# Performance work log

Measured on AMD Instinct MI355X. Metric: run time of the kernel, lower is better.

The kernel has to match this reference:

```python
import jax, jax.numpy as jnp
import numpy as np

N = 100000      # nodes
E = 1600000     # edges (avg degree 16)
IN = 512        # input feature dim
H, C = 8, 8     # conv1: 8 heads x 8 channels (hardcoded in module)
HID = H * C     # 64
OUT = 64        # output classes (conv2: 1 head, no concat)
NEG_SLOPE = 0.2 # PyG GATConv default leaky-relu slope


def setup_inputs() -> dict:
    key = jax.random.key(0)
    ks = jax.random.split(key, 10)
    x = jax.random.normal(ks[0], (N, IN), dtype=jnp.float32)
    edge_index = jax.random.randint(ks[1], (2, E), 0, N, dtype=jnp.int32)
    W1 = jax.random.normal(ks[2], (IN, HID), dtype=jnp.float32) / np.sqrt(IN).astype(np.float32)
    a_src1 = jax.random.normal(ks[3], (H, C), dtype=jnp.float32) * 0.1
    a_dst1 = jax.random.normal(ks[4], (H, C), dtype=jnp.float32) * 0.1
    b1 = jnp.zeros((HID,), dtype=jnp.float32)
    W2 = jax.random.normal(ks[5], (HID, OUT), dtype=jnp.float32) / np.sqrt(HID).astype(np.float32)
    a_src2 = jax.random.normal(ks[6], (1, OUT), dtype=jnp.float32) * 0.1
    a_dst2 = jax.random.normal(ks[7], (1, OUT), dtype=jnp.float32) * 0.1
    b2 = jnp.zeros((OUT,), dtype=jnp.float32)
    return {"x": x, "edge_index": edge_index, "W1": W1, "a_src1": a_src1,
            "a_dst1": a_dst1, "b1": b1, "W2": W2, "a_src2": a_src2,
            "a_dst2": a_dst2, "b2": b2}


def _gat_attend(h, src, dst, a_s, a_d, n_nodes):
    """h: [N,H,C]; src/dst: [E]; a_s/a_d: [H,C] -> aggregated [N,H,C]."""
    # per-node half-scores (PyG decomposition of a^T [Wx_i || Wx_j])
    sc_s = jnp.sum(h * a_s, axis=-1)                       # [N,H]
    sc_d = jnp.sum(h * a_d, axis=-1)                       # [N,H]
    logits = jax.nn.leaky_relu(sc_s[src] + sc_d[dst], NEG_SLOPE)  # [E,H]
    # segment softmax over edges grouped by destination node
    mx = jax.ops.segment_max(logits, dst, num_segments=n_nodes)   # [N,H]
    ex = jnp.exp(logits - mx[dst])                          # [E,H]
    denom = jax.ops.segment_sum(ex, dst, num_segments=n_nodes)    # [N,H]
    alpha = ex / (denom[dst] + 1e-16)                       # [E,H]
    msg = h[src] * alpha[:, :, None]                        # [E,H,C]
    return jax.ops.segment_sum(msg, dst, num_segments=n_nodes)    # [N,H,C]


def reference(x, edge_index, W1, a_src1, a_dst1, b1, W2, a_src2, a_dst2, b2):
    n = x.shape[0]
    loop = jnp.arange(n, dtype=edge_index.dtype)
    src = jnp.concatenate([edge_index[0], loop])            # self-loops (PyG default)
    dst = jnp.concatenate([edge_index[1], loop])
    # conv1: 8 heads, concat
    h1 = (x @ W1).reshape(n, H, C)
    o1 = _gat_attend(h1, src, dst, a_src1, a_dst1, n).reshape(n, HID) + b1
    x2 = jax.nn.elu(o1)
    # conv2: 1 head, no concat
    h2 = (x2 @ W2).reshape(n, 1, OUT)
    o2 = _gat_attend(h2, src, dst, a_src2, a_dst2, n)[:, 0] + b2
    return jax.nn.log_softmax(o2, axis=1)
```

## Files before the change

### kernel.cpp

```cpp
#include <hip/hip_runtime.h>
#include <cstdint>
#include <cstddef>

#define LEAKY 0.2f
#define NEG_INF -3.402823466e38f
static const int CHUNK = 2048;

typedef __attribute__((ext_vector_type(8))) short short8;
typedef __attribute__((ext_vector_type(4))) float floatx4;

__device__ __forceinline__ float dot4(float4 a, float4 b) {
    return a.x * b.x + a.y * b.y + a.z * b.z + a.w * b.w;
}

__device__ __forceinline__ unsigned short f2bf(float f) {
    unsigned u = __float_as_uint(f);
    u += 0x7fffu + ((u >> 16) & 1u);
    return (unsigned short)(u >> 16);
}
__device__ __forceinline__ float bf2f(unsigned short u) {
    return __uint_as_float(((unsigned)u) << 16);
}

__global__ __launch_bounds__(256) void k_init_deg(int* __restrict__ deg, int Nn) {
    int i = blockIdx.x * 256 + threadIdx.x;
    if (i < Nn) deg[i] = 1;
}

__global__ __launch_bounds__(256) void k_count_p(const int* __restrict__ ei, int* __restrict__ deg,
                                                 int E, int Nn) {
    int part = blockIdx.x & 7;
    int lo = (int)((long long)Nn * part >> 3);
    int hi = (int)((long long)Nn * (part + 1) >> 3);
    int nthr = (gridDim.x >> 3) * 256;
    int tid = (blockIdx.x >> 3) * 256 + threadIdx.x;
    for (int e = tid; e < E; e += nthr) {
        int d = ei[E + e];
        if (d >= lo && d < hi) atomicAdd(&deg[d], 1);
    }
}

__global__ __launch_bounds__(256) void k_scan1(const int* __restrict__ deg, int* __restrict__ bsum, int Nn) {
    __shared__ int sm[256];
    int b = blockIdx.x, t = threadIdx.x;
    int s = 0;
    int i0 = b * CHUNK + t * 8;
#pragma unroll
    for (int j = 0; j < 8; ++j) { int i = i0 + j; if (i < Nn) s += deg[i]; }
    sm[t] = s;
    __syncthreads();
    for (int o = 128; o; o >>= 1) { if (t < o) sm[t] += sm[t + o]; __syncthreads(); }
    if (t == 0) bsum[b] = sm[0];
}

__global__ void k_scan2(const int* __restrict__ bsum, int* __restrict__ bpre, int B) {
    int l = threadIdx.x;
    int v = (l < B) ? bsum[l] : 0;
    int inc = v;
#pragma unroll
    for (int o = 1; o < 64; o <<= 1) { int u = __shfl_up(inc, o); if (l >= o) inc += u; }
    if (l < B) bpre[l] = inc - v;
}

__global__ __launch_bounds__(256) void k_scan3(const int* __restrict__ deg, const int* __restrict__ bpre,
                                               int* __restrict__ indptr, int* __restrict__ cursor, int Nn) {
    __shared__ int wsum[4];
    int b = blockIdx.x, t = threadIdx.x, lane = t & 63, w = t >> 6;
    int i0 = b * CHUNK + t * 8;
    int d[8]; int s = 0;
#pragma unroll
    for (int j = 0; j < 8; ++j) { int i = i0 + j; d[j] = (i < Nn) ? deg[i] : 0; s += d[j]; }
    int inc = s;
#pragma unroll
    for (int o = 1; o < 64; o <<= 1) { int u = __shfl_up(inc, o); if (lane >= o) inc += u; }
    if (lane == 63) wsum[w] = inc;
    __syncthreads();
    int wofs = 0;
    for (int k = 0; k < w; ++k) wofs += wsum[k];
    int base = bpre[b] + wofs + (inc - s);
    int run = 0;
#pragma unroll
    for (int j = 0; j < 8; ++j) {
        int i = i0 + j;
        if (i < Nn) {
            int v = base + run;
            indptr[i] = v; cursor[i] = v;
            run += d[j];
            if (i == Nn - 1) indptr[Nn] = v + d[j];
        }
    }
}

__global__ __launch_bounds__(256) void k_fill_p(const int* __restrict__ ei, int* __restrict__ cursor,
                                                int* __restrict__ csr, int E, int Nn) {
    int part = blockIdx.x & 7;
    int lo = (int)((long long)Nn * part >> 3);
    int hi = (int)((long long)Nn * (part + 1) >> 3);
    int nthr = (gridDim.x >> 3) * 256;
    int tid = (blockIdx.x >> 3) * 256 + threadIdx.x;
    int tot = E + Nn;
    for (int idx = tid; idx < tot; idx += nthr) {
        int d = (idx < E) ? ei[E + idx] : idx - E;
        if (d >= lo && d < hi) {
            int s = (idx < E) ? ei[idx] : idx - E;
            int slot = atomicAdd(&cursor[d], 1);
            csr[slot] = s;
        }
    }
}

__global__ __launch_bounds__(256) void k_prepW(const float* __restrict__ W1, unsigned short* __restrict__ W1t) {
    int i = blockIdx.x * 256 + threadIdx.x;
    if (i >= 64 * 512) return;
    int n = i >> 9, k = i & 511;
    W1t[i] = f2bf(W1[k * 64 + n]);
}

__global__ __launch_bounds__(256) void gemm1_mfma(const float* __restrict__ A, const unsigned short* __restrict__ W1t,
                                                  unsigned short* __restrict__ C, int M) {
    __shared__ __align__(16) unsigned short As[128][40];
    __shared__ __align__(16) unsigned short Bs[64][40];
    int t = threadIdx.x;
    int w = t >> 6, l = t & 63;
    int quad = l >> 4, lm = l & 15;
    int row0 = blockIdx.x * 128;

    floatx4 acc[2][4] = {};

    for (int k0 = 0; k0 < 512; k0 += 32) {
#pragma unroll
        for (int j = 0; j < 4; ++j) {
            int f = t + 256 * j;
            int r = f >> 3, c4 = f & 7;
            int rg = row0 + r; if (rg >= M) rg = M - 1;
            float4 v = *(const float4*)(A + (size_t)rg * 512 + k0 + c4 * 4);
            ushort4 b; b.x = f2bf(v.x); b.y = f2bf(v.y); b.z = f2bf(v.z); b.w = f2bf(v.w);
            *(ushort4*)&As[r][c4 * 4] = b;
        }
        {
            int n = t >> 2, seg = t & 3;
            *(uint4*)&Bs[n][seg * 8] = *(const uint4*)(W1t + (size_t)n * 512 + k0 + seg * 8);
        }
        __syncthreads();

        short8 af[2], bfm[4];
#pragma unroll
        for (int tm = 0; tm < 2; ++tm) {
            int m = w * 32 + tm * 16 + lm;
            af[tm] = *(const short8*)&As[m][quad * 8];
        }
#pragma unroll
        for (int tn = 0; tn < 4; ++tn) {
            int n = tn * 16 + lm;
            bfm[tn] = *(const short8*)&Bs[n][quad * 8];
        }
#pragma unroll
        for (int tm = 0; tm < 2; ++tm)
#pragma unroll
            for (int tn = 0; tn < 4; ++tn)
                acc[tm][tn] = __builtin_amdgcn_mfma_f32_16x16x32_bf16(af[tm], bfm[tn], acc[tm][tn], 0, 0, 0);
        __syncthreads();
    }

#pragma unroll
    for (int tm = 0; tm < 2; ++tm) {
#pragma unroll
        for (int r = 0; r < 4; ++r) {
            int row = row0 + w * 32 + tm * 16 + quad * 4 + r;
            if (row < M) {
#pragma unroll
                for (int tn = 0; tn < 4; ++tn)
                    C[(size_t)row * 64 + tn * 16 + lm] = f2bf(acc[tm][tn][r]);
            }
        }
    }
}

template <int KB>
__global__ __launch_bounds__(256) void gemm_n64(const float* __restrict__ A, const float* __restrict__ B,
                                                unsigned short* __restrict__ C, int M, int K) {
    __shared__ float As[KB][68];
    __shared__ float Bs[KB][68];
    int tid = threadIdx.x;
    int row0 = blockIdx.x * 64;
    int tx = tid & 15, ty = tid >> 4;
    float acc[4][4] = {};
    for (int k0 = 0; k0 < K; k0 += KB) {
#pragma unroll
        for (int j = 0; j < (64 * KB) / (256 * 4); ++j) {
            int f = tid + 256 * j;
            int r = f / (KB / 4);
            int c4 = f % (KB / 4);
            int rg = row0 + r; if (rg >= M) rg = M - 1;
            float4 v = *(const float4*)(A + (size_t)rg * K + k0 + c4 * 4);
            As[c4 * 4 + 0][r] = v.x; As[c4 * 4 + 1][r] = v.y;
            As[c4 * 4 + 2][r] = v.z; As[c4 * 4 + 3][r] = v.w;
        }
#pragma unroll
        for (int j = 0; j < (KB * 64) / (256 * 4); ++j) {
            int f = tid + 256 * j;
            int kk = f / 16, c4 = f % 16;
            *(float4*)&Bs[kk][c4 * 4] = *(const float4*)(B + (size_t)(k0 + kk) * 64 + c4 * 4);
        }
        __syncthreads();
#pragma unroll
        for (int kk = 0; kk < KB; ++kk) {
            float4 a = *(const float4*)&As[kk][ty * 4];
            float4 b = *(const float4*)&Bs[kk][tx * 4];
            float av[4] = {a.x, a.y, a.z, a.w};
            float bv[4] = {b.x, b.y, b.z, b.w};
#pragma unroll
            for (int i = 0; i < 4; ++i)
#pragma unroll
                for (int j = 0; j < 4; ++j) acc[i][j] += av[i] * bv[j];
        }
        __syncthreads();
    }
#pragma unroll
    for (int i = 0; i < 4; ++i) {
        int rg = row0 + ty * 4 + i;
        if (rg < M) {
            ushort4 b; b.x = f2bf(acc[i][0]); b.y = f2bf(acc[i][1]);
            b.z = f2bf(acc[i][2]); b.w = f2bf(acc[i][3]);
            *(ushort4*)(C + (size_t)rg * 64 + tx * 4) = b;
        }
    }
}

__global__ __launch_bounds__(256) void k_sc1(const unsigned short* __restrict__ h1, const float* __restrict__ as1,
                                             const float* __restrict__ ad1, float* __restrict__ scs,
                                             float* __restrict__ scd, int Nn) {
    int i = blockIdx.x * 256 + threadIdx.x;
    if (i >= Nn * 8) return;
    int h = i & 7;
    ushort4 p0 = *(const ushort4*)(h1 + (size_t)i * 8);
    ushort4 p1 = *(const ushort4*)(h1 + (size_t)i * 8 + 4);
    float4 v0 = make_float4(bf2f(p0.x), bf2f(p0.y), bf2f(p0.z), bf2f(p0.w));
    float4 v1 = make_float4(bf2f(p1.x), bf2f(p1.y), bf2f(p1.z), bf2f(p1.w));
    const float4* asp = (const float4*)(as1 + h * 8);
    const float4* adp = (const float4*)(ad1 + h * 8);
    scs[i] = dot4(v0, asp[0]) + dot4(v1, asp[1]);
    scd[i] = dot4(v0, adp[0]) + dot4(v1, adp[1]);
}

__global__ __launch_bounds__(256) void k_sc2(const unsigned short* __restrict__ h2, const float* __restrict__ as2,
                                             const float* __restrict__ ad2, float* __restrict__ scs,
                                             float* __restrict__ scd, int Nn) {
    int wave = (blockIdx.x * 256 + threadIdx.x) >> 6;
    int lane = threadIdx.x & 63;
    if (wave >= Nn) return;
    float v = bf2f(h2[(size_t)wave * 64 + lane]);
    float ss = v * as2[lane], sd = v * ad2[lane];
#pragma unroll
    for (int o = 32; o; o >>= 1) { ss += __shfl_xor(ss, o); sd += __shfl_xor(sd, o); }
    if (lane == 0) { scs[wave] = ss; scd[wave] = sd; }
}

__global__ __launch_bounds__(256) void k_agg1(const unsigned short* __restrict__ h1, const float* __restrict__ scs,
                                              const float* __restrict__ scd, const int* __restrict__ indptr,
                                              const int* __restrict__ csr, const float* __restrict__ b1,
                                              float* __restrict__ x2, int Nn) {
    int node = (blockIdx.x * 256 + threadIdx.x) >> 6;
    int l = threadIdx.x & 63;
    if (node >= Nn) return;
    int h8 = l & 7, grp = l >> 3;
    int sub = l >> 5, c2 = l & 31;
    int head2 = c2 >> 2;
    int start = indptr[node], end = indptr[node + 1];
    float sd = scd[node * 8 + h8];

    float mx = NEG_INF;
    for (int base = start; base < end; base += 8) {
        int slot = base + grp;
        int s = csr[slot < end ? slot : start];
        float v = scs[s * 8 + h8] + sd;
        v = v > 0.f ? v : LEAKY * v;
        mx = fmaxf(mx, (slot < end) ? v : NEG_INF);
    }
#pragma unroll
    for (int o = 8; o < 64; o <<= 1) mx = fmaxf(mx, __shfl_xor(mx, o));

    float dsum = 0.f, acc0 = 0.f, acc1 = 0.f;
    for (int base = start; base < end; base += 64) {
        int e = base + l;
        int s64 = csr[e < end ? e : start];
        int cnt = min(64, end - base);
        int nb = (cnt + 7) >> 3;
        for (int b = 0; b < nb; ++b) {
            int slot = base + b * 8 + grp;
            int sb = __shfl(s64, b * 8 + grp);
            float v = scs[sb * 8 + h8] + sd;
            v = v > 0.f ? v : LEAKY * v;
            float ex = (slot < end) ? __expf(v - mx) : 0.f;
            dsum += ex;
#pragma unroll
            for (int j = 0; j < 8; j += 2) {
                int jj = j + sub;
                float exv = __shfl(ex, (jj << 3) | head2);
                int s = __shfl(s64, b * 8 + jj);
                unsigned hp = *(const unsigned*)(h1 + (size_t)s * 64 + c2 * 2);
                acc0 += exv * bf2f((unsigned short)(hp & 0xffffu));
                acc1 += exv * bf2f((unsigned short)(hp >> 16));
            }
        }
    }
#pragma unroll
    for (int o = 8; o < 64; o <<= 1) dsum += __shfl_xor(dsum, o);
    acc0 += __shfl_xor(acc0, 32);
    acc1 += __shfl_xor(acc1, 32);
    float dh = __shfl(dsum, head2);
    float inv = 1.f / (dh + 1e-16f);

    float o0 = acc0 * inv + b1[c2 * 2];
    float o1 = acc1 * inv + b1[c2 * 2 + 1];
    o0 = o0 > 0.f ? o0 : expm1f(o0);
    o1 = o1 > 0.f ? o1 : expm1f(o1);
    if (sub == 0) {
        float2 r = make_float2(o0, o1);
        *(float2*)&x2[(size_t)node * 64 + c2 * 2] = r;
    }
}

__global__ __launch_bounds__(256) void k_agg2(const unsigned short* __restrict__ h2, const float* __restrict__ scs,
                                              const float* __restrict__ scd, const int* __restrict__ indptr,
                                              const int* __restrict__ csr, const float* __restrict__ b2,
                                              float* __restrict__ out, int Nn) {
    int node = (blockIdx.x * 256 + threadIdx.x) >> 6;
    int l = threadIdx.x & 63;
    if (node >= Nn) return;
    int sub = l >> 5, c2 = l & 31;
    int start = indptr[node], end = indptr[node + 1];
    float sd = scd[node];

    float mx = NEG_INF;
    for (int base = start; base < end; base += 64) {
        int e = base + l;
        int s = csr[e < end ? e : start];
        float v = scs[s] + sd;
        v = v > 0.f ? v : LEAKY * v;
        mx = fmaxf(mx, (e < end) ? v : NEG_INF);
    }
#pragma unroll
    for (int o = 32; o; o >>= 1) mx = fmaxf(mx, __shfl_xor(mx, o));

    float dsum = 0.f, acc0 = 0.f, acc1 = 0.f;
    for (int base = start; base < end; base += 64) {
        int e = base + l;
        int s64 = csr[e < end ? e : start];
        float v = scs[s64] + sd;
        v = v > 0.f ? v : LEAKY * v;
        float ex = (e < end) ? __expf(v - mx) : 0.f;
        dsum += ex;
        int cnt = min(64, end - base);
        for (int j = 0; j < cnt; j += 2) {
            int jj = j + sub;
            float exv = __shfl(ex, jj);
            int s = __shfl(s64, jj);
            unsigned hp = *(const unsigned*)(h2 + (size_t)s * 64 + c2 * 2);
            acc0 += exv * bf2f((unsigned short)(hp & 0xffffu));
            acc1 += exv * bf2f((unsigned short)(hp >> 16));
        }
    }
#pragma unroll
    for (int o = 32; o; o >>= 1) dsum += __shfl_xor(dsum, o);
    acc0 += __shfl_xor(acc0, 32);
    acc1 += __shfl_xor(acc1, 32);
    float inv = 1.f / (dsum + 1e-16f);
    float o0 = acc0 * inv + b2[c2 * 2];
    float o1 = acc1 * inv + b2[c2 * 2 + 1];

    float m2 = fmaxf(o0, o1);
#pragma unroll
    for (int d = 16; d; d >>= 1) m2 = fmaxf(m2, __shfl_xor(m2, d));
    float e0 = __expf(o0 - m2), e1 = __expf(o1 - m2);
    float se = e0 + e1;
#pragma unroll
    for (int d = 16; d; d >>= 1) se += __shfl_xor(se, d);
    float ls = __logf(se);
    if (sub == 0) {
        float2 r = make_float2(o0 - m2 - ls, o1 - m2 - ls);
        *(float2*)&out[(size_t)node * 64 + c2 * 2] = r;
    }
}

extern "C" void kernel_launch(void* const* d_in, const int* in_sizes, int n_in,
                              void* d_out, int out_size, void* d_ws, size_t ws_size,
                              hipStream_t stream) {
    (void)n_in; (void)out_size; (void)ws_size;
    const float* x   = (const float*)d_in[0];
    const int*   ei  = (const int*)d_in[1];
    const float* W1  = (const float*)d_in[2];
    const float* as1 = (const float*)d_in[3];
    const float* ad1 = (const float*)d_in[4];
    const float* b1  = (const float*)d_in[5];
    const float* W2  = (const float*)d_in[6];
    const float* as2 = (const float*)d_in[7];
    const float* ad2 = (const float*)d_in[8];
    const float* b2  = (const float*)d_in[9];
    float* out = (float*)d_out;

    const int N = in_sizes[0] / 512;
    const int E = in_sizes[1] / 2;

    char* p = (char*)d_ws;
    auto alloc = [&](size_t bytes) -> char* {
        char* r = p; p += (bytes + 255) & ~(size_t)255; return r;
    };
    unsigned short* h1bf = (unsigned short*)alloc((size_t)N * 64 * 2);
    float* x2    = (float*)alloc((size_t)N * 64 * 4);
    unsigned short* h2bf = h1bf;
    float* sc1s  = (float*)alloc((size_t)N * 8 * 4);
    float* sc1d  = (float*)alloc((size_t)N * 8 * 4);
    float* sc2s  = (float*)alloc((size_t)N * 4);
    float* sc2d  = (float*)alloc((size_t)N * 4);
    int*   deg   = (int*)alloc((size_t)N * 4);
    int*   cursor= (int*)alloc((size_t)N * 4);
    int*   indptr= (int*)alloc((size_t)(N + 1) * 4);
    int*   csr   = (int*)alloc((size_t)(E + N) * 4);
    int*   bsum  = (int*)alloc(64 * 4);
    int*   bpre  = (int*)alloc(64 * 4);
    unsigned short* W1t = (unsigned short*)alloc(64 * 512 * 2);

    const int B = (N + CHUNK - 1) / CHUNK;

    k_init_deg<<<(N + 255) / 256, 256, 0, stream>>>(deg, N);
    k_count_p<<<1024, 256, 0, stream>>>(ei, deg, E, N);
    k_scan1  <<<B, 256, 0, stream>>>(deg, bsum, N);
    k_scan2  <<<1, 64, 0, stream>>>(bsum, bpre, B);
    k_scan3  <<<B, 256, 0, stream>>>(deg, bpre, indptr, cursor, N);
    k_fill_p <<<1024, 256, 0, stream>>>(ei, cursor, csr, E, N);

    k_prepW<<<(64 * 512 + 255) / 256, 256, 0, stream>>>(W1, W1t);
    gemm1_mfma<<<(N + 127) / 128, 256, 0, stream>>>(x, W1t, h1bf, N);
    k_sc1 <<<(N * 8 + 255) / 256, 256, 0, stream>>>(h1bf, as1, ad1, sc1s, sc1d, N);
    k_agg1<<<(N + 3) / 4, 256, 0, stream>>>(h1bf, sc1s, sc1d, indptr, csr, b1, x2, N);

    gemm_n64<64><<<(N + 63) / 64, 256, 0, stream>>>(x2, W2, h2bf, N, 64);
    k_sc2 <<<(N + 3) / 4, 256, 0, stream>>>(h2bf, as2, ad2, sc2s, sc2d, N);
    k_agg2<<<(N + 3) / 4, 256, 0, stream>>>(h2bf, sc2s, sc2d, indptr, csr, b2, out, N);
}
```

Baseline: 672.0 us.

## Gather 16-byte bf16 feature rows per lane in GAT aggregation kernels

Both aggregation kernels change their lane mapping. Each lane now loads a uint4 holding 8 bf16 channels of one neighbour, so a wave covers 8 edges per step, where before each lane loaded a 4-byte pair and the wave walked edges two at a time. This cuts the number of gather instructions and shuffles per edge. In exchange it needs 8 accumulators per lane, a cross-group butterfly reduction at the end, and a rewritten log-softmax epilogue over 8-lane groups. It also raises register pressure.

New measurement: 655.3 us. 1.03x faster.

```diff
diff --git a/kernel.cpp b/kernel.cpp
--- a/kernel.cpp
+++ b/kernel.cpp
@@ -21,6 +21,8 @@
 __device__ __forceinline__ float bf2f(unsigned short u) {
     return __uint_as_float(((unsigned)u) << 16);
 }
+__device__ __forceinline__ float bflo(unsigned u) { return __uint_as_float(u << 16); }
+__device__ __forceinline__ float bfhi(unsigned u) { return __uint_as_float(u & 0xffff0000u); }
 
 __global__ __launch_bounds__(256) void k_init_deg(int* __restrict__ deg, int Nn) {
     int i = blockIdx.x * 256 + threadIdx.x;
@@ -264,8 +266,6 @@
     int l = threadIdx.x & 63;
     if (node >= Nn) return;
     int h8 = l & 7, grp = l >> 3;
-    int sub = l >> 5, c2 = l & 31;
-    int head2 = c2 >> 2;
     int start = indptr[node], end = indptr[node + 1];
     float sd = scd[node * 8 + h8];
 
@@ -280,12 +280,14 @@
 #pragma unroll
     for (int o = 8; o < 64; o <<= 1) mx = fmaxf(mx, __shfl_xor(mx, o));
 
-    float dsum = 0.f, acc0 = 0.f, acc1 = 0.f;
+    float dsum = 0.f;
+    float acc8[8] = {};
     for (int base = start; base < end; base += 64) {
         int e = base + l;
         int s64 = csr[e < end ? e : start];
         int cnt = min(64, end - base);
         int nb = (cnt + 7) >> 3;
+#pragma unroll 2
         for (int b = 0; b < nb; ++b) {
             int slot = base + b * 8 + grp;
             int sb = __shfl(s64, b * 8 + grp);
@@ -293,31 +295,34 @@
             v = v > 0.f ? v : LEAKY * v;
             float ex = (slot < end) ? __expf(v - mx) : 0.f;
             dsum += ex;
-#pragma unroll
-            for (int j = 0; j < 8; j += 2) {
-                int jj = j + sub;
-                float exv = __shfl(ex, (jj << 3) | head2);
-                int s = __shfl(s64, b * 8 + jj);
-                unsigned hp = *(const unsigned*)(h1 + (size_t)s * 64 + c2 * 2);
-                acc0 += exv * bf2f((unsigned short)(hp & 0xffffu));
-                acc1 += exv * bf2f((unsigned short)(hp >> 16));
-            }
-        }
-    }
-#pragma unroll
-    for (int o = 8; o < 64; o <<= 1) dsum += __shfl_xor(dsum, o);
-    acc0 += __shfl_xor(acc0, 32);
-    acc1 += __shfl_xor(acc1, 32);
-    float dh = __shfl(dsum, head2);
-    float inv = 1.f / (dh + 1e-16f);
-
-    float o0 = acc0 * inv + b1[c2 * 2];
-    float o1 = acc1 * inv + b1[c2 * 2 + 1];
-    o0 = o0 > 0.f ? o0 : expm1f(o0);
-    o1 = o1 > 0.f ? o1 : expm1f(o1);
-    if (sub == 0) {
-        float2 r = make_float2(o0, o1);
-        *(float2*)&x2[(size_t)node * 64 + c2 * 2] = r;
+            uint4 q = *(const uint4*)(h1 + (size_t)sb * 64 + h8 * 8);
+            acc8[0] += ex * bflo(q.x); acc8[1] += ex * bfhi(q.x);
+            acc8[2] += ex * bflo(q.y); acc8[3] += ex * bfhi(q.y);
+            acc8[4] += ex * bflo(q.z); acc8[5] += ex * bfhi(q.z);
+            acc8[6] += ex * bflo(q.w); acc8[7] += ex * bfhi(q.w);
+        }
+    }
+#pragma unroll
+    for (int o = 8; o < 64; o <<= 1) {
+        dsum += __shfl_xor(dsum, o);
+#pragma unroll
+        for (int k = 0; k < 8; ++k) acc8[k] += __shfl_xor(acc8[k], o);
+    }
+    if (grp == 0) {
+        float inv = 1.f / (dsum + 1e-16f);
+        float4 ba = *((const float4*)b1 + h8 * 2);
+        float4 bb = *((const float4*)b1 + h8 * 2 + 1);
+        float o0 = acc8[0] * inv + ba.x, o1 = acc8[1] * inv + ba.y;
+        float o2 = acc8[2] * inv + ba.z, o3 = acc8[3] * inv + ba.w;
+        float o4 = acc8[4] * inv + bb.x, o5 = acc8[5] * inv + bb.y;
+        float o6 = acc8[6] * inv + bb.z, o7 = acc8[7] * inv + bb.w;
+        o0 = o0 > 0.f ? o0 : expm1f(o0); o1 = o1 > 0.f ? o1 : expm1f(o1);
+        o2 = o2 > 0.f ? o2 : expm1f(o2); o3 = o3 > 0.f ? o3 : expm1f(o3);
+        o4 = o4 > 0.f ? o4 : expm1f(o4); o5 = o5 > 0.f ? o5 : expm1f(o5);
+        o6 = o6 > 0.f ? o6 : expm1f(o6); o7 = o7 > 0.f ? o7 : expm1f(o7);
+        float* dst = x2 + (size_t)node * 64 + h8 * 8;
+        *(float4*)dst = make_float4(o0, o1, o2, o3);
+        *(float4*)(dst + 4) = make_float4(o4, o5, o6, o7);
     }
 }
 
@@ -328,7 +333,7 @@
     int node = (blockIdx.x * 256 + threadIdx.x) >> 6;
     int l = threadIdx.x & 63;
     if (node >= Nn) return;
-    int sub = l >> 5, c2 = l & 31;
+    int g = l >> 3, c8 = l & 7;
     int start = indptr[node], end = indptr[node + 1];
     float sd = scd[node];
 
@@ -343,7 +348,8 @@
 #pragma unroll
     for (int o = 32; o; o >>= 1) mx = fmaxf(mx, __shfl_xor(mx, o));
 
-    float dsum = 0.f, acc0 = 0.f, acc1 = 0.f;
+    float dsum = 0.f;
+    float acc8[8] = {};
     for (int base = start; base < end; base += 64) {
         int e = base + l;
         int s64 = csr[e < end ? e : start];
@@ -352,34 +358,49 @@
         float ex = (e < end) ? __expf(v - mx) : 0.f;
         dsum += ex;
         int cnt = min(64, end - base);
-        for (int j = 0; j < cnt; j += 2) {
-            int jj = j + sub;
-            float exv = __shfl(ex, jj);
-            int s = __shfl(s64, jj);
-            unsigned hp = *(const unsigned*)(h2 + (size_t)s * 64 + c2 * 2);
-            acc0 += exv * bf2f((unsigned short)(hp & 0xffffu));
-            acc1 += exv * bf2f((unsigned short)(hp >> 16));
+        int nb = (cnt + 7) >> 3;
+#pragma unroll 2
+        for (int b = 0; b < nb; ++b) {
+            float exv = __shfl(ex, b * 8 + g);
+            int sb = __shfl(s64, b * 8 + g);
+            uint4 q = *(const uint4*)(h2 + (size_t)sb * 64 + c8 * 8);
+            acc8[0] += exv * bflo(q.x); acc8[1] += exv * bfhi(q.x);
+            acc8[2] += exv * bflo(q.y); acc8[3] += exv * bfhi(q.y);
+            acc8[4] += exv * bflo(q.z); acc8[5] += exv * bfhi(q.z);
+            acc8[6] += exv * bflo(q.w); acc8[7] += exv * bfhi(q.w);
         }
     }
 #pragma unroll
     for (int o = 32; o; o >>= 1) dsum += __shfl_xor(dsum, o);
-    acc0 += __shfl_xor(acc0, 32);
-    acc1 += __shfl_xor(acc1, 32);
+#pragma unroll
+    for (int o = 8; o < 64; o <<= 1)
+#pragma unroll
+        for (int k = 0; k < 8; ++k) acc8[k] += __shfl_xor(acc8[k], o);
+
     float inv = 1.f / (dsum + 1e-16f);
-    float o0 = acc0 * inv + b2[c2 * 2];
-    float o1 = acc1 * inv + b2[c2 * 2 + 1];
-
-    float m2 = fmaxf(o0, o1);
-#pragma unroll
-    for (int d = 16; d; d >>= 1) m2 = fmaxf(m2, __shfl_xor(m2, d));
-    float e0 = __expf(o0 - m2), e1 = __expf(o1 - m2);
-    float se = e0 + e1;
-#pragma unroll
-    for (int d = 16; d; d >>= 1) se += __shfl_xor(se, d);
-    float ls = __logf(se);
-    if (sub == 0) {
-        float2 r = make_float2(o0 - m2 - ls, o1 - m2 - ls);
-        *(float2*)&out[(size_t)node * 64 + c2 * 2] = r;
+    float4 ba = *((const float4*)b2 + c8 * 2);
+    float4 bb = *((const float4*)b2 + c8 * 2 + 1);
+    float ov[8];
+    ov[0] = acc8[0] * inv + ba.x; ov[1] = acc8[1] * inv + ba.y;
+    ov[2] = acc8[2] * inv + ba.z; ov[3] = acc8[3] * inv + ba.w;
+    ov[4] = acc8[4] * inv + bb.x; ov[5] = acc8[5] * inv + bb.y;
+    ov[6] = acc8[6] * inv + bb.z; ov[7] = acc8[7] * inv + bb.w;
+
+    float m2 = ov[0];
+#pragma unroll
+    for (int k = 1; k < 8; ++k) m2 = fmaxf(m2, ov[k]);
+#pragma unroll
+    for (int o = 1; o < 8; o <<= 1) m2 = fmaxf(m2, __shfl_xor(m2, o));
+    float se = 0.f;
+#pragma unroll
+    for (int k = 0; k < 8; ++k) se += __expf(ov[k] - m2);
+#pragma unroll
+    for (int o = 1; o < 8; o <<= 1) se += __shfl_xor(se, o);
+    float ls = m2 + __logf(se);
+    if (g == 0) {
+        float* dst = out + (size_t)node * 64 + c8 * 8;
+        *(float4*)dst = make_float4(ov[0] - ls, ov[1] - ls, ov[2] - ls, ov[3] - ls);
+        *(float4*)(dst + 4) = make_float4(ov[4] - ls, ov[5] - ls, ov[6] - ls, ov[7] - ls);
     }
 }
 
```
